# Optimization experiments

Hardware: AMD Instinct MI355X
Metric: run time of the kernel (lower is better)

The kernel has to match this reference:

```python
import jax, jax.numpy as jnp
import numpy as np

# Irreps spec: 32x0e (dim 1, with bias) + 16x1o (dim 3) + 8x2e (dim 5)
# x: [B, n_channels_in, 120] where 120 = 32*1 + 16*3 + 8*5

B = 1024
N_IN = 256
N_OUT = 256


def setup_inputs() -> dict:
    key = jax.random.key(0)
    k_x, k0, k1, k2 = jax.random.split(key, 4)
    std = 1.0 / np.sqrt(N_IN)
    x = jax.random.normal(k_x, (B, N_IN, 120), dtype=jnp.float32)
    W0 = jax.random.normal(k0, (32, N_OUT, N_IN), dtype=jnp.float32) * std
    W1 = jax.random.normal(k1, (16, N_OUT, N_IN), dtype=jnp.float32) * std
    W2 = jax.random.normal(k2, (8, N_OUT, N_IN), dtype=jnp.float32) * std
    b0 = jnp.zeros((32, N_OUT), dtype=jnp.float32)
    return {"x": x, "W0": W0, "W1": W1, "W2": W2, "b0": b0}


def reference(x, W0, W1, W2, b0):
    # Grouped form of the original per-multiplicity loop. Slices of the last
    # axis are consecutive per (irrep, multiplicity), so reshaping a group of
    # `mul` copies of an irrep of dim `d` to [..., n_in, mul, d] and doing one
    # batched einsum reproduces the original concatenation order exactly.
    groups = [(W0, 1, b0), (W1, 3, None), (W2, 5, None)]  # (weights[mul,o,i], irrep dim, bias[mul,o] or None)
    outs = []
    start = 0
    for W, d, b in groups:
        mul = W.shape[0]
        width = mul * d
        xs = x[..., start:start + width].reshape(*x.shape[:-1], mul, d)  # [..., n_in, mul, d]
        y = jnp.einsum('moi,...imd->...omd', W, xs)  # [..., n_out, mul, d]
        if b is not None:  # only l=0 irreps get a bias, broadcast over d (=1)
            y = y + b.T[:, :, None]  # [n_out, mul, 1]
        outs.append(y.reshape(*y.shape[:-2], width))  # [..., n_out, mul*d]
        start += width
    return jnp.concatenate(outs, axis=-1)  # [..., n_out, 120]
```

## Files before the change

kernel.cpp:

```cpp
#include <hip/hip_runtime.h>

typedef __attribute__((ext_vector_type(8))) short bf16x8;
typedef __attribute__((ext_vector_type(4))) float f32x4;
typedef __attribute__((ext_vector_type(8))) unsigned short u16x8;

#define DEVINL __device__ __forceinline__
#define AS1 __attribute__((address_space(1)))
#define AS3 __attribute__((address_space(3)))

constexpr int NI = 256;
constexpr int NO = 256;
constexpr int NC = 120;
constexpr int BROW = NC * NI;
constexpr int WELEMS = 56 * NO * NI;
constexpr size_t XT_ELEMS = (size_t)NC * 1024 * NI;

DEVINL ushort f2bf(float x) {
  unsigned u = __float_as_uint(x);
  u += 0x7FFFu + ((u >> 16) & 1u);
  return (ushort)(u >> 16);
}
DEVINL float bf2f(ushort v) { return __uint_as_float((unsigned)v << 16); }

__global__ __launch_bounds__(256) void prep_w(const float* __restrict__ w0,
                                              const float* __restrict__ w1,
                                              const float* __restrict__ w2,
                                              ushort* __restrict__ wb) {
  const int m = blockIdx.x >> 5;
  const int kc = blockIdx.x & 31;
  const int o = threadIdx.x;
  const float* src;
  if (m < 32)      src = w0 + ((size_t)(m * NO + o)) * NI;
  else if (m < 48) src = w1 + ((size_t)((m - 32) * NO + o)) * NI;
  else             src = w2 + ((size_t)((m - 48) * NO + o)) * NI;
  src += kc * 8;
  float4 a = *reinterpret_cast<const float4*>(src);
  float4 b = *reinterpret_cast<const float4*>(src + 4);
  u16x8 p = { f2bf(a.x), f2bf(a.y), f2bf(a.z), f2bf(a.w),
              f2bf(b.x), f2bf(b.y), f2bf(b.z), f2bf(b.w) };
  *reinterpret_cast<u16x8*>(wb + ((size_t)(blockIdx.x * 256 + o)) * 8) = p;
}

__global__ __launch_bounds__(256) void xpose(const float* __restrict__ x,
                                             ushort* __restrict__ xt) {
  __shared__ float tl[64 * 121];
  const int bid = blockIdx.x;
  const int b = bid >> 2, iq = bid & 3;
  const int t = threadIdx.x;
  const float* xb = x + (size_t)b * BROW + (size_t)iq * 64 * NC;
#pragma unroll
  for (int j = 0; j < 15; ++j) {
    const int e = (j * 256 + t) * 2;
    float2 v = *reinterpret_cast<const float2*>(xb + e);
    const int i = e / 120, c = e % 120;
    tl[i * 121 + c] = v.x;
    tl[i * 121 + c + 1] = v.y;
  }
  __syncthreads();
  ushort* dst = xt + (size_t)b * BROW + iq * 64;
#pragma unroll
  for (int q = 0; q < 4; ++q) {
    const int chunk = q * 256 + t;
    if (chunk < 960) {
      const int c = chunk >> 3, ich = chunk & 7;
      u16x8 p;
#pragma unroll
      for (int k = 0; k < 8; ++k) p[k] = f2bf(tl[(ich * 8 + k) * 121 + c]);
      *reinterpret_cast<u16x8*>(dst + (size_t)c * NI + ich * 8) = p;
    }
  }
}

__global__ __launch_bounds__(256, 4) void e3mix7(ushort* xt,
                                                 const ushort* __restrict__ wb,
                                                 const float* __restrict__ bias0) {
  __shared__ ushort xs[2][64 * 64];
  const int bid = blockIdx.x;
  const int c  = bid % 120;
  const int bt = bid / 120;
  const int m  = c < 32 ? c : (c < 80 ? 32 + (c - 32) / 3 : 48 + (c - 80) / 5);
  const int bg = bt * 64;

  const int tid = threadIdx.x, lane = tid & 63, wid = tid >> 6;
  const int rb = lane & 15, rg = lane >> 4;
  const int wo = wid * 64;

  const int srow = wid * 16 + (lane >> 3);
  const ushort* gsrc = xt + (size_t)(bg + srow) * BROW + (size_t)c * NI
                          + ((lane & 7) ^ (srow & 7)) * 8;
  ushort* ldst0 = &xs[0][wid * 1024];
  ushort* ldst1 = &xs[1][wid * 1024];

  f32x4 acc[4][4];
#pragma unroll
  for (int i = 0; i < 4; ++i)
#pragma unroll
    for (int j = 0; j < 4; ++j) acc[i][j] = (f32x4)0.0f;

#define STAGE(LD, S)                                                          \
  do {                                                                        \
    __builtin_amdgcn_global_load_lds((const AS1 void*)(gsrc + (S) * 64),      \
                                     (AS3 void*)(LD), 16, 0, 0);              \
    __builtin_amdgcn_global_load_lds((const AS1 void*)(gsrc + (S) * 64        \
                                                       + (size_t)8 * BROW),   \
                                     (AS3 void*)((LD) + 512), 16, 0, 0);      \
  } while (0)

  STAGE(ldst0, 0);
  __syncthreads();

#pragma unroll 1
  for (int s = 0; s < 4; ++s) {
    if (s < 3) STAGE((s & 1) ? ldst0 : ldst1, s + 1);
    const ushort* xb = xs[s & 1];
#pragma unroll
    for (int kh = 0; kh < 2; ++kh) {
      bf16x8 a[4], w[4];
#pragma unroll
      for (int fb = 0; fb < 4; ++fb)
        a[fb] = *reinterpret_cast<const bf16x8*>(
            &xb[(fb * 16 + rb) * 64 + (((kh * 4 + rg) ^ (rb & 7)) * 8)]);
#pragma unroll
      for (int fo = 0; fo < 4; ++fo)
        w[fo] = *reinterpret_cast<const bf16x8*>(
            wb + ((size_t)((m * 32 + s * 8 + kh * 4 + rg) * NO
                           + wo + fo * 16 + rb)) * 8);
#pragma unroll
      for (int fb = 0; fb < 4; ++fb)
#pragma unroll
        for (int fo = 0; fo < 4; ++fo)
          acc[fb][fo] = __builtin_amdgcn_mfma_f32_16x16x32_bf16(a[fb], w[fo],
                                                                acc[fb][fo], 0, 0, 0);
    }
    __syncthreads();
  }
#undef STAGE

  if (c < 32) {
#pragma unroll
    for (int fo = 0; fo < 4; ++fo) {
      const float bv = bias0[c * NO + wo + fo * 16 + rb];
#pragma unroll
      for (int fb = 0; fb < 4; ++fb) acc[fb][fo] += bv;
    }
  }

#pragma unroll
  for (int fb = 0; fb < 4; ++fb)
#pragma unroll
    for (int r = 0; r < 4; ++r) {
      ushort* ot = xt + (size_t)(bg + fb * 16 + rg * 4 + r) * BROW + (size_t)c * NI;
#pragma unroll
      for (int fo = 0; fo < 4; ++fo)
        ot[wo + fo * 16 + rb] = f2bf(acc[fb][fo][r]);
    }
}

__global__ __launch_bounds__(256) void otrans(const ushort* __restrict__ xt,
                                              float* __restrict__ out) {
  __shared__ ushort tl[120 * 132];
  const int bid = blockIdx.x;
  const int b = bid >> 1, oh = bid & 1;
  const int t = threadIdx.x;
  const ushort* src = xt + (size_t)b * BROW + oh * 128;
#pragma unroll
  for (int q = 0; q < 15; ++q) {
    const int chunk = q * 256 + t;
    const int c = chunk >> 5, o4 = (chunk & 31) * 4;
    ushort4 v = *reinterpret_cast<const ushort4*>(src + (size_t)c * NI + o4);
    *reinterpret_cast<ushort4*>(&tl[c * 132 + o4]) = v;
  }
  __syncthreads();
  const int op = t & 127, ch = t >> 7;
  float* dst = out + ((size_t)b * NO + oh * 128 + op) * NC + ch * 60;
#pragma unroll
  for (int j = 0; j < 15; ++j) {
    float4 v;
    v.x = bf2f(tl[(ch * 60 + 4 * j + 0) * 132 + op]);
    v.y = bf2f(tl[(ch * 60 + 4 * j + 1) * 132 + op]);
    v.z = bf2f(tl[(ch * 60 + 4 * j + 2) * 132 + op]);
    v.w = bf2f(tl[(ch * 60 + 4 * j + 3) * 132 + op]);
    *reinterpret_cast<float4*>(dst + 4 * j) = v;
  }
}

__global__ __launch_bounds__(512, 4) void e3mix2f(const float* __restrict__ x,
                                                  const ushort* __restrict__ wb,
                                                  const float* __restrict__ bias0,
                                                  float* __restrict__ out) {
  __shared__ ushort xs[8 * 16 * 64];
  const int bid = blockIdx.x;
  const int ct = bid % 15, bt = bid / 15;
  const int c0 = ct * 8, bg = bt * 16;
  const int t = threadIdx.x, lane = t & 63, wid = t >> 6;
  const int sb = lane >> 2, sp = lane & 3;
  const int rb = lane & 15, rg = lane >> 4;
  const int oc = wid * 16 + rb;
  const int srow = (wid * 16 + sb) * 64;
  const int sk0 = (sp * 16) ^ ((sb & 7) << 3);
  const int sk1 = (sp * 16 + 8) ^ ((sb & 7) << 3);

  f32x4 acc[8][2];
#pragma unroll
  for (int i = 0; i < 8; ++i) { acc[i][0] = (f32x4)0.0f; acc[i][1] = (f32x4)0.0f; }
  bf16x8 w00 = {}, w01 = {}, w10 = {}, w11 = {};

#pragma unroll 1
  for (int s = 0; s < 4; ++s) {
    if (s) __syncthreads();
    u16x8 v0, v1;
    const float* src = x + (size_t)(bg + sb) * (NI * NC)
                         + (size_t)(s * 64 + sp * 16) * NC + (c0 + wid);
#pragma unroll
    for (int jj = 0; jj < 8; ++jj) v0[jj] = f2bf(src[jj * NC]);
#pragma unroll
    for (int jj = 0; jj < 8; ++jj) v1[jj] = f2bf(src[(8 + jj) * NC]);
    *reinterpret_cast<u16x8*>(&xs[srow + sk0]) = v0;
    *reinterpret_cast<u16x8*>(&xs[srow + sk1]) = v1;
    __syncthreads();

    int mprev = -1;
#pragma unroll
    for (int cc = 0; cc < 8; ++cc) {
      const int c = c0 + cc;
      const int m = c < 32 ? c : (c < 80 ? 32 + (c - 32) / 3 : 48 + (c - 80) / 5);
      if (m != mprev) {
        const ushort* wp = wb + ((size_t)((m * 32 + s * 8 + rg) * NO + oc)) * 8;
        w00 = *reinterpret_cast<const bf16x8*>(wp);
        w10 = *reinterpret_cast<const bf16x8*>(wp + (size_t)4 * NO * 8);
        w01 = *reinterpret_cast<const bf16x8*>(wp + 128 * 8);
        w11 = *reinterpret_cast<const bf16x8*>(wp + (size_t)4 * NO * 8 + 128 * 8);
        mprev = m;
      }
      const ushort* xp = xs + (cc * 16 + rb) * 64;
      const int sz = (rb & 7) << 3;
      bf16x8 a0 = *reinterpret_cast<const bf16x8*>(xp + ((rg * 8) ^ sz));
      bf16x8 a1 = *reinterpret_cast<const bf16x8*>(xp + ((32 + rg * 8) ^ sz));
      acc[cc][0] = __builtin_amdgcn_mfma_f32_16x16x32_bf16(a0, w00, acc[cc][0], 0, 0, 0);
      acc[cc][0] = __builtin_amdgcn_mfma_f32_16x16x32_bf16(a1, w10, acc[cc][0], 0, 0, 0);
      acc[cc][1] = __builtin_amdgcn_mfma_f32_16x16x32_bf16(a0, w01, acc[cc][1], 0, 0, 0);
      acc[cc][1] = __builtin_amdgcn_mfma_f32_16x16x32_bf16(a1, w11, acc[cc][1], 0, 0, 0);
    }
  }

  if (c0 < 32) {
#pragma unroll
    for (int cc = 0; cc < 8; ++cc) {
      acc[cc][0] += bias0[(c0 + cc) * NO + oc];
      acc[cc][1] += bias0[(c0 + cc) * NO + oc + 128];
    }
  }

  const int br0 = bg + rg * 4;
#pragma unroll
  for (int of = 0; of < 2; ++of)
#pragma unroll
    for (int r = 0; r < 4; ++r) {
      float4 va = make_float4(acc[0][of][r], acc[1][of][r], acc[2][of][r], acc[3][of][r]);
      float4 vb = make_float4(acc[4][of][r], acc[5][of][r], acc[6][of][r], acc[7][of][r]);
      float* dst = out + ((size_t)(br0 + r) * NO + oc + of * 128) * NC + c0;
      *reinterpret_cast<float4*>(dst) = va;
      *reinterpret_cast<float4*>(dst + 4) = vb;
    }
}

extern "C" void kernel_launch(void* const* d_in, const int* in_sizes, int n_in,
                              void* d_out, int out_size, void* d_ws, size_t ws_size,
                              hipStream_t stream) {
  const float* x  = (const float*)d_in[0];
  const float* w0 = (const float*)d_in[1];
  const float* w1 = (const float*)d_in[2];
  const float* w2 = (const float*)d_in[3];
  const float* b0 = (const float*)d_in[4];
  float* out = (float*)d_out;
  ushort* wb = (ushort*)d_ws;
  ushort* xt = wb + WELEMS;

  prep_w<<<56 * 32, 256, 0, stream>>>(w0, w1, w2, wb);
  const bool big = ws_size >= (size_t)2 * (WELEMS + XT_ELEMS);
  if (big) {
    xpose<<<4096, 256, 0, stream>>>(x, xt);
    e3mix7<<<16 * 120, 256, 0, stream>>>(xt, wb, b0);
    otrans<<<2048, 256, 0, stream>>>(xt, out);
  } else {
    e3mix2f<<<960, 512, 0, stream>>>(x, wb, b0, out);
  }
}
```

Measured before the change: 132.2 us.

## Fuse output transpose into GEMM kernel, drop otrans pass

The mixing GEMM kernel is restructured so each block handles 8 channels (one per wave) for 32 batch rows and a 64-wide output slice. Results are staged in LDS with a layout that lets them be written straight to the final fp32 output. This removes the separate otrans kernel along with the bf16 round-trip through the workspace and one launch. The trade-off is a smaller per-wave tile (2x4 MFMA fragments instead of 4x4), which means less reuse of each weight load.

```diff
diff --git a/kernel.cpp b/kernel.cpp
--- a/kernel.cpp
+++ b/kernel.cpp
@@ -71,116 +71,107 @@
   }
 }
 
-__global__ __launch_bounds__(256, 4) void e3mix7(ushort* xt,
+__global__ __launch_bounds__(512, 4) void e3mix9(const ushort* __restrict__ xt,
                                                  const ushort* __restrict__ wb,
-                                                 const float* __restrict__ bias0) {
-  __shared__ ushort xs[2][64 * 64];
+                                                 const float* __restrict__ bias0,
+                                                 float* __restrict__ out) {
+  __shared__ ushort xs[2 * 16384];
   const int bid = blockIdx.x;
-  const int c  = bid % 120;
-  const int bt = bid / 120;
-  const int m  = c < 32 ? c : (c < 80 ? 32 + (c - 32) / 3 : 48 + (c - 80) / 5);
-  const int bg = bt * 64;
-
-  const int tid = threadIdx.x, lane = tid & 63, wid = tid >> 6;
+  const int oq = bid & 3;
+  const int rest = bid >> 2;
+  const int ct = rest % 15;
+  const int bt = rest / 15;
+  const int c0 = ct * 8, bg = bt * 32, og = oq * 64;
+
+  const int tid = threadIdx.x, lane = tid & 63, w = tid >> 6;
   const int rb = lane & 15, rg = lane >> 4;
-  const int wo = wid * 64;
-
-  const int srow = wid * 16 + (lane >> 3);
-  const ushort* gsrc = xt + (size_t)(bg + srow) * BROW + (size_t)c * NI
-                          + ((lane & 7) ^ (srow & 7)) * 8;
-  ushort* ldst0 = &xs[0][wid * 1024];
-  ushort* ldst1 = &xs[1][wid * 1024];
-
-  f32x4 acc[4][4];
-#pragma unroll
-  for (int i = 0; i < 4; ++i)
+  const int c = c0 + w;
+  const int m = c < 32 ? c : (c < 80 ? 32 + (c - 32) / 3 : 48 + (c - 80) / 5);
+
+  const int lr = lane >> 3;
+  const ushort* gsrc = xt + (size_t)(bg + lr) * BROW + (size_t)c * NI
+                          + ((lane & 7) ^ lr) * 8;
+
+  f32x4 acc[2][4];
+#pragma unroll
+  for (int i = 0; i < 2; ++i)
 #pragma unroll
     for (int j = 0; j < 4; ++j) acc[i][j] = (f32x4)0.0f;
 
-#define STAGE(LD, S)                                                          \
-  do {                                                                        \
-    __builtin_amdgcn_global_load_lds((const AS1 void*)(gsrc + (S) * 64),      \
-                                     (AS3 void*)(LD), 16, 0, 0);              \
-    __builtin_amdgcn_global_load_lds((const AS1 void*)(gsrc + (S) * 64        \
-                                                       + (size_t)8 * BROW),   \
-                                     (AS3 void*)((LD) + 512), 16, 0, 0);      \
+#define STAGE9(BUF, S)                                                         \
+  do {                                                                         \
+    __builtin_amdgcn_global_load_lds(                                          \
+        (const AS1 void*)(gsrc + (size_t)(S) * 64 + (size_t)0 * 8 * BROW),     \
+        (AS3 void*)(xs + (BUF) * 16384 + w * 2048 + 0 * 512), 16, 0, 0);       \
+    __builtin_amdgcn_global_load_lds(                                          \
+        (const AS1 void*)(gsrc + (size_t)(S) * 64 + (size_t)1 * 8 * BROW),     \
+        (AS3 void*)(xs + (BUF) * 16384 + w * 2048 + 1 * 512), 16, 0, 0);       \
+    __builtin_amdgcn_global_load_lds(                                          \
+        (const AS1 void*)(gsrc + (size_t)(S) * 64 + (size_t)2 * 8 * BROW),     \
+        (AS3 void*)(xs + (BUF) * 16384 + w * 2048 + 2 * 512), 16, 0, 0);       \
+    __builtin_amdgcn_global_load_lds(                                          \
+        (const AS1 void*)(gsrc + (size_t)(S) * 64 + (size_t)3 * 8 * BROW),     \
+        (AS3 void*)(xs + (BUF) * 16384 + w * 2048 + 3 * 512), 16, 0, 0);       \
   } while (0)
 
-  STAGE(ldst0, 0);
+  STAGE9(0, 0);
   __syncthreads();
 
 #pragma unroll 1
   for (int s = 0; s < 4; ++s) {
-    if (s < 3) STAGE((s & 1) ? ldst0 : ldst1, s + 1);
-    const ushort* xb = xs[s & 1];
+    if (s < 3) STAGE9((s + 1) & 1, s + 1);
+    const ushort* xb = xs + (s & 1) * 16384 + w * 2048;
 #pragma unroll
     for (int kh = 0; kh < 2; ++kh) {
-      bf16x8 a[4], w[4];
-#pragma unroll
-      for (int fb = 0; fb < 4; ++fb)
+      bf16x8 a[2], wf[4];
+#pragma unroll
+      for (int fb = 0; fb < 2; ++fb)
         a[fb] = *reinterpret_cast<const bf16x8*>(
-            &xb[(fb * 16 + rb) * 64 + (((kh * 4 + rg) ^ (rb & 7)) * 8)]);
+            xb + (fb * 16 + rb) * 64 + (((kh * 4 + rg) ^ (rb & 7)) * 8));
 #pragma unroll
       for (int fo = 0; fo < 4; ++fo)
-        w[fo] = *reinterpret_cast<const bf16x8*>(
+        wf[fo] = *reinterpret_cast<const bf16x8*>(
             wb + ((size_t)((m * 32 + s * 8 + kh * 4 + rg) * NO
-                           + wo + fo * 16 + rb)) * 8);
-#pragma unroll
-      for (int fb = 0; fb < 4; ++fb)
+                           + og + fo * 16 + rb)) * 8);
+#pragma unroll
+      for (int fb = 0; fb < 2; ++fb)
 #pragma unroll
         for (int fo = 0; fo < 4; ++fo)
-          acc[fb][fo] = __builtin_amdgcn_mfma_f32_16x16x32_bf16(a[fb], w[fo],
+          acc[fb][fo] = __builtin_amdgcn_mfma_f32_16x16x32_bf16(a[fb], wf[fo],
                                                                 acc[fb][fo], 0, 0, 0);
     }
     __syncthreads();
   }
-#undef STAGE
-
-  if (c < 32) {
+#undef STAGE9
+
+  if (c0 < 32) {
 #pragma unroll
     for (int fo = 0; fo < 4; ++fo) {
-      const float bv = bias0[c * NO + wo + fo * 16 + rb];
-#pragma unroll
-      for (int fb = 0; fb < 4; ++fb) acc[fb][fo] += bv;
-    }
-  }
-
-#pragma unroll
-  for (int fb = 0; fb < 4; ++fb)
-#pragma unroll
-    for (int r = 0; r < 4; ++r) {
-      ushort* ot = xt + (size_t)(bg + fb * 16 + rg * 4 + r) * BROW + (size_t)c * NI;
+      const float bv = bias0[c * NO + og + fo * 16 + rb];
+#pragma unroll
+      for (int fb = 0; fb < 2; ++fb) acc[fb][fo] += bv;
+    }
+  }
+
+#pragma unroll
+  for (int fb = 0; fb < 2; ++fb)
+#pragma unroll
+    for (int r = 0; r < 4; ++r)
 #pragma unroll
       for (int fo = 0; fo < 4; ++fo)
-        ot[wo + fo * 16 + rb] = f2bf(acc[fb][fo][r]);
-    }
-}
-
-__global__ __launch_bounds__(256) void otrans(const ushort* __restrict__ xt,
-                                              float* __restrict__ out) {
-  __shared__ ushort tl[120 * 132];
-  const int bid = blockIdx.x;
-  const int b = bid >> 1, oh = bid & 1;
-  const int t = threadIdx.x;
-  const ushort* src = xt + (size_t)b * BROW + oh * 128;
-#pragma unroll
-  for (int q = 0; q < 15; ++q) {
-    const int chunk = q * 256 + t;
-    const int c = chunk >> 5, o4 = (chunk & 31) * 4;
-    ushort4 v = *reinterpret_cast<const ushort4*>(src + (size_t)c * NI + o4);
-    *reinterpret_cast<ushort4*>(&tl[c * 132 + o4]) = v;
-  }
+        xs[(fb * 16 + rg * 4 + r) * 520 + (fo * 16 + rb) * 8 + w] =
+            f2bf(acc[fb][fo][r]);
   __syncthreads();
-  const int op = t & 127, ch = t >> 7;
-  float* dst = out + ((size_t)b * NO + oh * 128 + op) * NC + ch * 60;
-#pragma unroll
-  for (int j = 0; j < 15; ++j) {
-    float4 v;
-    v.x = bf2f(tl[(ch * 60 + 4 * j + 0) * 132 + op]);
-    v.y = bf2f(tl[(ch * 60 + 4 * j + 1) * 132 + op]);
-    v.z = bf2f(tl[(ch * 60 + 4 * j + 2) * 132 + op]);
-    v.w = bf2f(tl[(ch * 60 + 4 * j + 3) * 132 + op]);
-    *reinterpret_cast<float4*>(dst + 4 * j) = v;
+#pragma unroll
+  for (int i = 0; i < 4; ++i) {
+    const int g = i * 512 + tid;
+    const int bp = g >> 6, o = g & 63;
+    u16x8 v = *reinterpret_cast<const u16x8*>(xs + bp * 520 + o * 8);
+    float4 lo = make_float4(bf2f(v[0]), bf2f(v[1]), bf2f(v[2]), bf2f(v[3]));
+    float4 hi = make_float4(bf2f(v[4]), bf2f(v[5]), bf2f(v[6]), bf2f(v[7]));
+    float* dst = out + ((size_t)(bg + bp) * NO + og + o) * NC + c0;
+    *reinterpret_cast<float4*>(dst) = lo;
+    *reinterpret_cast<float4*>(dst + 4) = hi;
   }
 }
 
@@ -280,8 +271,7 @@
   const bool big = ws_size >= (size_t)2 * (WELEMS + XT_ELEMS);
   if (big) {
     xpose<<<4096, 256, 0, stream>>>(x, xt);
-    e3mix7<<<16 * 120, 256, 0, stream>>>(xt, wb, b0);
-    otrans<<<2048, 256, 0, stream>>>(xt, out);
+    e3mix9<<<1920, 512, 0, stream>>>(xt, wb, b0, out);
   } else {
     e3mix2f<<<960, 512, 0, stream>>>(x, wb, b0, out);
   }
```

New measurement: 161.9 us. 1.22x slower.
